# Performance work log

Hardware: AMD Instinct MI355X
Metric: run time of the kernel (lower is better)

Reference implementation:

```python
import jax, jax.numpy as jnp
import numpy as np

MARGIN = 0.5
EPS = 1e-6  # torch F.pairwise_distance adds eps to the difference: ||x1 - x2 + eps||

B, C, D = 262144, 100, 128


def setup_inputs() -> dict:
    key = jax.random.key(0)
    k1, k2, k3 = jax.random.split(key, 3)
    features = jax.random.normal(k1, (B, D), dtype=jnp.float32)
    prototypes = jax.random.normal(k2, (C, D), dtype=jnp.float32)
    labels = jax.random.randint(k3, (B,), 0, C, dtype=jnp.int64)
    return {"features": features, "prototypes": prototypes, "labels": labels}


def _l2_normalize(x, axis=-1, eps=1e-12):
    # matches torch F.normalize: x / max(||x||, eps)
    n = jnp.sqrt(jnp.sum(x * x, axis=axis, keepdims=True))
    return x / jnp.maximum(n, eps)


def reference(features, prototypes, labels):
    f = _l2_normalize(features, axis=1)        # [B, D]
    p = _l2_normalize(prototypes, axis=1)      # [C, D]
    Bn, Dn = f.shape
    Cn = p.shape[0]

    # ||f_i - p_j + EPS||^2 = ||f_i||^2 + ||p_j||^2 - 2 f_i.p_j
    #                         + 2*EPS*(sum(f_i) - sum(p_j)) + D*EPS^2
    dot = f @ p.T                              # [B, C]
    f2 = jnp.sum(f * f, axis=1)                # [B]
    p2 = jnp.sum(p * p, axis=1)                # [C]
    sf = jnp.sum(f, axis=1)                    # [B]
    sp = jnp.sum(p, axis=1)                    # [C]
    d2 = (f2[:, None] + p2[None, :] - 2.0 * dot
          + 2.0 * EPS * (sf[:, None] - sp[None, :])
          + Dn * (EPS * EPS))                  # [B, C]
    dists = jnp.sqrt(jnp.maximum(d2, 1e-12))   # [B, C]

    d_pos = jnp.take_along_axis(dists, labels[:, None], axis=1)  # [B, 1]
    hinge = jax.nn.relu(d_pos - dists + MARGIN)                  # [B, C]
    neg_mask = jnp.arange(Cn)[None, :] != labels[:, None]        # [B, C]
    # per-sample mean over the C-1 negative prototypes, then mean over batch
    per_sample = jnp.sum(jnp.where(neg_mask, hinge, 0.0), axis=1) / (Cn - 1)
    return jnp.mean(per_sample)
```

## Files before the change

### kernel.cpp

```cpp
#include <hip/hip_runtime.h>
#include <hip/hip_bf16.h>
#include <math.h>

#define DD 128
#define CC 100
#define NPAD 112
#define NT 7
#define MARGIN_F 0.5f
#define EPS_F 1e-6f
#define RW 16
#define CH 4
#define BROWS 256
#define NFRAG (NT * 4)

typedef __attribute__((ext_vector_type(8))) short bf16x8;
typedef __attribute__((ext_vector_type(4))) float f32x4;

__device__ __forceinline__ float fsqrt_f(float x) { return __builtin_amdgcn_sqrtf(x); }
__device__ __forceinline__ float frcp_f(float x)  { return __builtin_amdgcn_rcpf(x); }

__device__ __forceinline__ short f2bf(float x) {
    __hip_bfloat16 h = __float2bfloat16(x);
    return *reinterpret_cast<short*>(&h);
}

__global__ void prep_kernel(const float* __restrict__ p,
                            float* __restrict__ cj,
                            bf16x8* __restrict__ pnb,
                            float* __restrict__ out) {
    int j = blockIdx.x, tid = threadIdx.x;
    if (j == 0 && tid == 0) out[0] = -MARGIN_F / (float)(CC - 1);

    float inv = 0.0f;
    if (j < CC) {
        float a = p[j * DD + tid];
        float b = p[j * DD + tid + 64];
        float ss = a * a + b * b;
        float s1 = a + b;
#pragma unroll
        for (int off = 1; off < 64; off <<= 1) {
            ss += __shfl_xor(ss, off);
            s1 += __shfl_xor(s1, off);
        }
        inv = 1.0f / fmaxf(sqrtf(ss), 1e-12f);
        if (tid == 0) cj[j] = ss * inv * inv - 2.0f * EPS_F * (s1 * inv);
    } else {
        if (tid == 0) cj[j] = 1e9f;
    }

    if (tid < 16) {
        int kk = tid >> 2, g = tid & 3;
        int frag = (j >> 4) * 4 + kk;
        int lane = g * 16 + (j & 15);
        bf16x8 o;
        if (j < CC) {
            const float* row = p + j * DD + kk * 32 + g * 8;
#pragma unroll
            for (int q = 0; q < 8; ++q) o[q] = f2bf(row[q] * inv);
        } else {
#pragma unroll
            for (int q = 0; q < 8; ++q) o[q] = 0;
        }
        pnb[frag * 64 + lane] = o;
    }
}

__global__ __launch_bounds__(256) void proto_main_kernel(
        const float* __restrict__ feat,
        const bf16x8* __restrict__ pnb,
        const float* __restrict__ cj,
        const int* __restrict__ labels,
        float* __restrict__ out,
        int Bn, float scale) {
    const int lane = threadIdx.x & 63;
    const int w = threadIdx.x >> 6;
    const int g = lane >> 4, m = lane & 15;
    const long blkbase = (long)blockIdx.x * BROWS;

    __shared__ bf16x8 pnl[NFRAG * 64];
    __shared__ float cjs[NPAD];
    __shared__ float red[4];

    float cjr[NT];
#pragma unroll
    for (int t = 0; t < NT; ++t) cjr[t] = cj[t * 16 + m];

    float4 va[8];
    int lab;
    {
        long row = blkbase + w * RW + m;
        long rs = row < Bn ? row : (long)(Bn - 1);
        lab = labels[rs];
        const float4* fp = (const float4*)(feat + rs * DD);
#pragma unroll
        for (int kk = 0; kk < 4; ++kk) {
            va[kk * 2]     = fp[kk * 8 + g * 2];
            va[kk * 2 + 1] = fp[kk * 8 + g * 2 + 1];
        }
    }

#pragma unroll
    for (int i = 0; i < NFRAG * 64 / 256; ++i)
        pnl[i * 256 + threadIdx.x] = pnb[i * 256 + threadIdx.x];
    if (threadIdx.x < NPAD) cjs[threadIdx.x] = cj[threadIdx.x];
    __syncthreads();

    float hsum = 0.f;

#pragma unroll
    for (int c = 0; c < CH; ++c) {
        float ss = 0.f, s1 = 0.f;
#pragma unroll
        for (int q = 0; q < 8; ++q) {
            float4 v = va[q];
            ss += v.x * v.x + v.y * v.y + v.z * v.z + v.w * v.w;
            s1 += v.x + v.y + v.z + v.w;
        }
        ss += __shfl_xor(ss, 16); ss += __shfl_xor(ss, 32);
        s1 += __shfl_xor(s1, 16); s1 += __shfl_xor(s1, 32);
        float inv = frcp_f(fmaxf(fsqrt_f(ss), 1e-12f));
        float cf = ss * inv * inv + 2.f * EPS_F * (s1 * inv)
                 + (float)DD * (EPS_F * EPS_F);
        float m2i = -2.f * inv;
        int labc = lab;

        bf16x8 afr[4];
#pragma unroll
        for (int kk = 0; kk < 4; ++kk) {
            float4 a = va[kk * 2], b = va[kk * 2 + 1];
            union { bf16x8 v; __hip_bfloat162 h[4]; } u;
            u.h[0] = __float22bfloat162_rn(make_float2(a.x, a.y));
            u.h[1] = __float22bfloat162_rn(make_float2(a.z, a.w));
            u.h[2] = __float22bfloat162_rn(make_float2(b.x, b.y));
            u.h[3] = __float22bfloat162_rn(make_float2(b.z, b.w));
            afr[kk] = u.v;
        }

        if (c + 1 < CH) {
            long nrow = blkbase + (c + 1) * 64 + w * RW + m;
            long nrs = nrow < Bn ? nrow : (long)(Bn - 1);
            lab = labels[nrs];
            const float4* fp = (const float4*)(feat + nrs * DD);
#pragma unroll
            for (int kk = 0; kk < 4; ++kk) {
                va[kk * 2]     = fp[kk * 8 + g * 2];
                va[kk * 2 + 1] = fp[kk * 8 + g * 2 + 1];
            }
        }

        float cf_r[4], m2i_r[4];
        int lab_r[4];
#pragma unroll
        for (int r = 0; r < 4; ++r) {
            int addr = (g * 4 + r) << 2;
            cf_r[r]  = __int_as_float(__builtin_amdgcn_ds_bpermute(addr, __float_as_int(cf)));
            m2i_r[r] = __int_as_float(__builtin_amdgcn_ds_bpermute(addr, __float_as_int(m2i)));
            lab_r[r] = __builtin_amdgcn_ds_bpermute(addr, labc);
        }
        float cjl_r[4];
#pragma unroll
        for (int r = 0; r < 4; ++r) cjl_r[r] = cjs[lab_r[r]];

        f32x4 accpos = (f32x4)0.f;
        {
            int lanehi = lane & 48;
            int fbase = (labc >> 4) << 2;
            int lsub  = lanehi + (labc & 15);
#pragma unroll
            for (int kk = 0; kk < 4; ++kk) {
                bf16x8 bp = pnl[(fbase + kk) * 64 + lsub];
                accpos = __builtin_amdgcn_mfma_f32_16x16x32_bf16(
                    afr[kk], bp, accpos, 0, 0, 0);
            }
        }
        float a01 = (lane & 1) ? accpos[1] : accpos[0];
        float a23 = (lane & 1) ? accpos[3] : accpos[2];
        float vsrc = (lane & 2) ? a23 : a01;
        float hb[4];
        {
            int hl = (lane >> 4) * 20;
#pragma unroll
            for (int r = 0; r < 4; ++r) {
                float dotp = __int_as_float(
                    __builtin_amdgcn_ds_bpermute((hl + r) << 2, __float_as_int(vsrc)));
                float d2p = fmaf(dotp, m2i_r[r], cf_r[r]) + cjl_r[r];
                float dpd = fsqrt_f(fmaxf(d2p, 1e-12f));
                long rr = blkbase + c * 64 + w * RW + g * 4 + r;
                hb[r] = (rr < (long)Bn) ? (dpd + MARGIN_F) : 0.f;
            }
        }

        f32x4 acc[NT];
#pragma unroll
        for (int t = 0; t < NT; ++t) acc[t] = (f32x4)0.f;
#pragma unroll
        for (int t = 0; t < NT; ++t) {
            bf16x8 bfr[4];
#pragma unroll
            for (int kk = 0; kk < 4; ++kk) bfr[kk] = pnl[(t * 4 + kk) * 64 + lane];
#pragma unroll
            for (int kk = 0; kk < 4; ++kk)
                acc[t] = __builtin_amdgcn_mfma_f32_16x16x32_bf16(
                    afr[kk], bfr[kk], acc[t], 0, 0, 0);
        }

        float ms0 = 0.f, ms1 = 0.f, ms2 = 0.f, ms3 = 0.f;
#pragma unroll
        for (int t = 0; t < NT; ++t) {
            float e0 = fmaf(acc[t][0], m2i_r[0], cf_r[0]);
            float e1 = fmaf(acc[t][1], m2i_r[1], cf_r[1]);
            float e2 = fmaf(acc[t][2], m2i_r[2], cf_r[2]);
            float e3 = fmaf(acc[t][3], m2i_r[3], cf_r[3]);
            ms0 += fminf(fsqrt_f(e0 + cjr[t]), hb[0]);
            ms1 += fminf(fsqrt_f(e1 + cjr[t]), hb[1]);
            ms2 += fminf(fsqrt_f(e2 + cjr[t]), hb[2]);
            ms3 += fminf(fsqrt_f(e3 + cjr[t]), hb[3]);
        }
        hsum += fmaf((float)NT, hb[0], -ms0);
        hsum += fmaf((float)NT, hb[1], -ms1);
        hsum += fmaf((float)NT, hb[2], -ms2);
        hsum += fmaf((float)NT, hb[3], -ms3);
    }

#pragma unroll
    for (int off = 32; off > 0; off >>= 1) hsum += __shfl_xor(hsum, off);
    if (lane == 0) red[w] = hsum;
    __syncthreads();
    if (threadIdx.x == 0)
        atomicAdd(out, (red[0] + red[1] + red[2] + red[3]) * scale);
}

extern "C" void kernel_launch(void* const* d_in, const int* in_sizes, int n_in,
                              void* d_out, int out_size, void* d_ws, size_t ws_size,
                              hipStream_t stream) {
    const float* feat   = (const float*)d_in[0];
    const float* prot   = (const float*)d_in[1];
    const int*   labels = (const int*)d_in[2];
    float* out = (float*)d_out;
    int Bn = in_sizes[0] / DD;

    bf16x8* pnb = (bf16x8*)d_ws;
    float* cjw  = (float*)((char*)d_ws + 28 * 64 * 16);

    prep_kernel<<<NPAD, 64, 0, stream>>>(prot, cjw, pnb, out);

    int blocks = (Bn + BROWS - 1) / BROWS;
    float scale = 1.0f / ((float)Bn * (float)(CC - 1));
    proto_main_kernel<<<blocks, 256, 0, stream>>>(feat, pnb, cjw, labels, out, Bn, scale);
}
```

Measured before the change: 40.03 us.

## Fuse prototype normalization into main kernel, drop separate prep launch

Removes the prep kernel and has every block of the main kernel normalize the prototypes, compute the per-class constants and build the bf16 MFMA fragments directly in shared memory. The output is cleared with a memset, and the label-side margin correction moves into each block's hinge sum. This removes one kernel launch and the serial dependency between prep and main. In exchange, each of the 1024 blocks redundantly reads the 51KB prototype matrix and does extra setup work with an added barrier.

```diff
diff --git a/kernel.cpp b/kernel.cpp
--- a/kernel.cpp
+++ b/kernel.cpp
@@ -24,66 +24,22 @@
     return *reinterpret_cast<short*>(&h);
 }
 
-__global__ void prep_kernel(const float* __restrict__ p,
-                            float* __restrict__ cj,
-                            bf16x8* __restrict__ pnb,
-                            float* __restrict__ out) {
-    int j = blockIdx.x, tid = threadIdx.x;
-    if (j == 0 && tid == 0) out[0] = -MARGIN_F / (float)(CC - 1);
-
-    float inv = 0.0f;
-    if (j < CC) {
-        float a = p[j * DD + tid];
-        float b = p[j * DD + tid + 64];
-        float ss = a * a + b * b;
-        float s1 = a + b;
-#pragma unroll
-        for (int off = 1; off < 64; off <<= 1) {
-            ss += __shfl_xor(ss, off);
-            s1 += __shfl_xor(s1, off);
-        }
-        inv = 1.0f / fmaxf(sqrtf(ss), 1e-12f);
-        if (tid == 0) cj[j] = ss * inv * inv - 2.0f * EPS_F * (s1 * inv);
-    } else {
-        if (tid == 0) cj[j] = 1e9f;
-    }
-
-    if (tid < 16) {
-        int kk = tid >> 2, g = tid & 3;
-        int frag = (j >> 4) * 4 + kk;
-        int lane = g * 16 + (j & 15);
-        bf16x8 o;
-        if (j < CC) {
-            const float* row = p + j * DD + kk * 32 + g * 8;
-#pragma unroll
-            for (int q = 0; q < 8; ++q) o[q] = f2bf(row[q] * inv);
-        } else {
-#pragma unroll
-            for (int q = 0; q < 8; ++q) o[q] = 0;
-        }
-        pnb[frag * 64 + lane] = o;
-    }
-}
-
 __global__ __launch_bounds__(256) void proto_main_kernel(
         const float* __restrict__ feat,
-        const bf16x8* __restrict__ pnb,
-        const float* __restrict__ cj,
+        const float* __restrict__ prot,
         const int* __restrict__ labels,
         float* __restrict__ out,
         int Bn, float scale) {
-    const int lane = threadIdx.x & 63;
-    const int w = threadIdx.x >> 6;
+    const int tid = threadIdx.x;
+    const int lane = tid & 63;
+    const int w = tid >> 6;
     const int g = lane >> 4, m = lane & 15;
     const long blkbase = (long)blockIdx.x * BROWS;
 
     __shared__ bf16x8 pnl[NFRAG * 64];
     __shared__ float cjs[NPAD];
+    __shared__ float invs[CC];
     __shared__ float red[4];
-
-    float cjr[NT];
-#pragma unroll
-    for (int t = 0; t < NT; ++t) cjr[t] = cj[t * 16 + m];
 
     float4 va[8];
     int lab;
@@ -99,11 +55,53 @@
         }
     }
 
-#pragma unroll
-    for (int i = 0; i < NFRAG * 64 / 256; ++i)
-        pnl[i * 256 + threadIdx.x] = pnb[i * 256 + threadIdx.x];
-    if (threadIdx.x < NPAD) cjs[threadIdx.x] = cj[threadIdx.x];
+    if (tid < 2 * CC) {
+        int j = tid >> 1, h = tid & 1;
+        const float4* pr = (const float4*)(prot + j * DD + h * 64);
+        float ss = 0.f, s1 = 0.f;
+#pragma unroll
+        for (int e = 0; e < 16; ++e) {
+            float4 v = pr[e];
+            ss += v.x * v.x + v.y * v.y + v.z * v.z + v.w * v.w;
+            s1 += v.x + v.y + v.z + v.w;
+        }
+        ss += __shfl_xor(ss, 1);
+        s1 += __shfl_xor(s1, 1);
+        float inv = 1.0f / fmaxf(sqrtf(ss), 1e-12f);
+        if (h == 0) {
+            invs[j] = inv;
+            cjs[j] = ss * inv * inv - 2.0f * EPS_F * (s1 * inv);
+        }
+    }
+    if (tid >= CC && tid < NPAD) cjs[tid] = 1e9f;
     __syncthreads();
+
+#pragma unroll
+    for (int i = 0; i < NFRAG * 64 / 256; ++i) {
+        int idx = i * 256 + tid;
+        int f = idx >> 6, l = idx & 63;
+        int n = (f >> 2) * 16 + (l & 15);
+        int kk = f & 3, k0 = kk * 32 + (l >> 4) * 8;
+        bf16x8 o;
+        if (n < CC) {
+            float inv = invs[n];
+            const float4* pr = (const float4*)(prot + n * DD + k0);
+            float4 a = pr[0], b = pr[1];
+            o[0] = f2bf(a.x * inv); o[1] = f2bf(a.y * inv);
+            o[2] = f2bf(a.z * inv); o[3] = f2bf(a.w * inv);
+            o[4] = f2bf(b.x * inv); o[5] = f2bf(b.y * inv);
+            o[6] = f2bf(b.z * inv); o[7] = f2bf(b.w * inv);
+        } else {
+#pragma unroll
+            for (int q = 0; q < 8; ++q) o[q] = 0;
+        }
+        pnl[idx] = o;
+    }
+    __syncthreads();
+
+    float cjr[NT];
+#pragma unroll
+    for (int t = 0; t < NT; ++t) cjr[t] = cjs[t * 16 + m];
 
     float hsum = 0.f;
 
@@ -186,7 +184,9 @@
                 float d2p = fmaf(dotp, m2i_r[r], cf_r[r]) + cjl_r[r];
                 float dpd = fsqrt_f(fmaxf(d2p, 1e-12f));
                 long rr = blkbase + c * 64 + w * RW + g * 4 + r;
-                hb[r] = (rr < (long)Bn) ? (dpd + MARGIN_F) : 0.f;
+                bool valid = rr < (long)Bn;
+                hb[r] = valid ? (dpd + MARGIN_F) : 0.f;
+                hsum -= valid ? (MARGIN_F * (1.0f / 16.0f)) : 0.f;
             }
         }
 
@@ -239,12 +239,9 @@
     float* out = (float*)d_out;
     int Bn = in_sizes[0] / DD;
 
-    bf16x8* pnb = (bf16x8*)d_ws;
-    float* cjw  = (float*)((char*)d_ws + 28 * 64 * 16);
-
-    prep_kernel<<<NPAD, 64, 0, stream>>>(prot, cjw, pnb, out);
+    hipMemsetAsync(d_out, 0, sizeof(float), stream);
 
     int blocks = (Bn + BROWS - 1) / BROWS;
     float scale = 1.0f / ((float)Bn * (float)(CC - 1));
-    proto_main_kernel<<<blocks, 256, 0, stream>>>(feat, pnb, cjw, labels, out, Bn, scale);
+    proto_main_kernel<<<blocks, 256, 0, stream>>>(feat, prot, labels, out, Bn, scale);
 }
```

New measurement: 48.09 us. +20.1%, slower.
